# Kernel optimization log

Hardware: AMD Instinct MI355X
Metric: run time of the kernel (lower is better)

## Reference

```python
import jax, jax.numpy as jnp
import numpy as np

H = 32  # hidden size, fixed by the source module


def setup_inputs() -> dict:
    key = jax.random.key(0)
    ks = jax.random.split(key, 11)
    B, T = 1024, 999
    s = 0.1  # weight init scale
    return {
        "input": jax.random.normal(ks[0], (B, T), jnp.float32),
        "W_ih1": jax.random.normal(ks[1], (4 * H, 1), jnp.float32) * s,
        "W_hh1": jax.random.normal(ks[2], (4 * H, H), jnp.float32) * s,
        "b_ih1": jax.random.normal(ks[3], (4 * H,), jnp.float32) * s,
        "b_hh1": jax.random.normal(ks[4], (4 * H,), jnp.float32) * s,
        "W_ih2": jax.random.normal(ks[5], (4 * H, H), jnp.float32) * s,
        "W_hh2": jax.random.normal(ks[6], (4 * H, H), jnp.float32) * s,
        "b_ih2": jax.random.normal(ks[7], (4 * H,), jnp.float32) * s,
        "b_hh2": jax.random.normal(ks[8], (4 * H,), jnp.float32) * s,
        "W_lin": jax.random.normal(ks[9], (1, H), jnp.float32) * s,
        "b_lin": jax.random.normal(ks[10], (1,), jnp.float32) * s,
        "future": 1000,
    }


def _lstm_cell(x, h, c, W_ih, W_hh, b_ih, b_hh):
    # PyTorch LSTMCell: gates = x@W_ih^T + b_ih + h@W_hh^T + b_hh, order i,f,g,o
    z = x @ W_ih.T + h @ W_hh.T + (b_ih + b_hh)
    i, f, g, o = jnp.split(z, 4, axis=-1)
    c_new = jax.nn.sigmoid(f) * c + jax.nn.sigmoid(i) * jnp.tanh(g)
    h_new = jax.nn.sigmoid(o) * jnp.tanh(c_new)
    return h_new, c_new


def reference(input, W_ih1, W_hh1, b_ih1, b_hh1, W_ih2, W_hh2, b_ih2, b_hh2,
              W_lin, b_lin, future):
    B = input.shape[0]
    dt = input.dtype
    z = jnp.zeros((B, H), dt)

    def step_tf(carry, x_t):  # teacher-forced phase, x_t: [B]
        h1, c1, h2, c2 = carry
        h1, c1 = _lstm_cell(x_t[:, None], h1, c1, W_ih1, W_hh1, b_ih1, b_hh1)
        h2, c2 = _lstm_cell(h1, h2, c2, W_ih2, W_hh2, b_ih2, b_hh2)
        out = h2 @ W_lin.T + b_lin  # [B,1]
        return (h1, c1, h2, c2), out[:, 0]

    carry, outs1 = jax.lax.scan(step_tf, (z, z, z, z), input.T)  # outs1: [T,B]

    def step_gen(carry, _):
        h1, c1, h2, c2, out = carry
        h1, c1 = _lstm_cell(out, h1, c1, W_ih1, W_hh1, b_ih1, b_hh1)
        h2, c2 = _lstm_cell(h1, h2, c2, W_ih2, W_hh2, b_ih2, b_hh2)
        out = h2 @ W_lin.T + b_lin
        return (h1, c1, h2, c2, out), out[:, 0]

    last_out = outs1[-1][:, None]
    _, outs2 = jax.lax.scan(step_gen, (*carry, last_out), None, length=future)

    return jnp.concatenate([outs1, outs2], axis=0).T  # [B, T+future]
```

## Files before the change

kernel.cpp:

```cpp
#include <hip/hip_runtime.h>

#define HH 32
#define LOG2E 1.44269504088896340736f
#define KCH 16

typedef float v2f __attribute__((ext_vector_type(2)));

#define DPPF(v, ctrl) \
    __int_as_float(__builtin_amdgcn_update_dpp(0, __float_as_int(v), (ctrl), 0xF, 0xF, true))
#define QP_B0 0x00
#define QP_B1 0x55
#define QP_B2 0xAA
#define QP_B3 0xFF
#define DPP_ROR4  0x124
#define DPP_ROR8  0x128
#define SWZ(v, pat) __int_as_float(__builtin_amdgcn_ds_swizzle(__float_as_int(v), (pat)))

__device__ __forceinline__ float hw_exp2(float x) {
    float r; asm("v_exp_f32 %0, %1" : "=v"(r) : "v"(x)); return r;
}
__device__ __forceinline__ float sigm_e(float z, float e) {
    return __builtin_amdgcn_rcpf(1.0f + hw_exp2(z * e));
}
__device__ __forceinline__ v2f pk_fma(v2f a, v2f b, v2f c) {
    return __builtin_elementwise_fma(a, b, c);
}
__device__ __forceinline__ void load_bc(const float* p, v2f* d) {
#pragma unroll
    for (int r = 0; r < 8; ++r) {
        float4 v = ((const float4*)p)[r];
        d[2*r]   = (v2f){v.x, v.y};
        d[2*r+1] = (v2f){v.z, v.w};
    }
}
__device__ __forceinline__ float out_reduce(float p) {
    p += DPPF(p, DPP_ROR4);
    p += DPPF(p, DPP_ROR8);
    p += SWZ(p, 0x401F);
    p += __shfl_xor(p, 32, 64);
    return p;
}

__global__ __launch_bounds__(128, 2)
void lstm_seq_kernel(const float* __restrict__ input,
                     const float* __restrict__ W_ih1, const float* __restrict__ W_hh1,
                     const float* __restrict__ b_ih1, const float* __restrict__ b_hh1,
                     const float* __restrict__ W_ih2, const float* __restrict__ W_hh2,
                     const float* __restrict__ b_ih2, const float* __restrict__ b_hh2,
                     const float* __restrict__ W_lin, const float* __restrict__ b_lin,
                     float* __restrict__ out, int T, int total)
{
    const int b    = blockIdx.x;
    const int tid  = threadIdx.x;
    const int w    = tid >> 6;
    const int lane = tid & 63;
    const int q    = lane & 3;
    const int ch   = lane >> 2;
    const int rowA = (q << 5) | ch;
    const int rowB = (q << 5) | (ch + 16);

    __shared__ __align__(16) float ring[2 * KCH * HH];
    __shared__ __align__(16) float h1x[HH];
    __shared__ __align__(16) float h2s[HH];
    __shared__ float xbuf;

    const bool  isg = (q == 2);
    const float es  = isg ? (-2.0f * LOG2E) : (-LOG2E);
    const float mm  = isg ? 2.0f : 1.0f;
    const float cc  = isg ? -1.0f : 0.0f;

    v2f m1A[16], m1B[16], m2A[16], m2B[16];
    float wxA = 0.f, wxB = 0.f, bA, bB, wlA = 0.f, wlB = 0.f, blin = 0.f;
    if (w == 0) {
        const v2f* pA = (const v2f*)(W_hh1 + rowA * HH);
        const v2f* pB = (const v2f*)(W_hh1 + rowB * HH);
#pragma unroll
        for (int r = 0; r < 16; ++r) { m1A[r] = pA[r]; m1B[r] = pB[r]; }
        wxA = W_ih1[rowA]; wxB = W_ih1[rowB];
        bA  = b_ih1[rowA] + b_hh1[rowA];
        bB  = b_ih1[rowB] + b_hh1[rowB];
    } else {
        const v2f* pA = (const v2f*)(W_ih2 + rowA * HH);
        const v2f* pB = (const v2f*)(W_ih2 + rowB * HH);
        const v2f* qA = (const v2f*)(W_hh2 + rowA * HH);
        const v2f* qB = (const v2f*)(W_hh2 + rowB * HH);
#pragma unroll
        for (int r = 0; r < 16; ++r) { m1A[r] = pA[r]; m1B[r] = pB[r];
                                       m2A[r] = qA[r]; m2B[r] = qB[r]; }
        bA  = b_ih2[rowA] + b_hh2[rowA];
        bB  = b_ih2[rowB] + b_hh2[rowB];
        wlA = W_lin[ch]; wlB = W_lin[ch + 16]; blin = b_lin[0];
    }

    float cA = 0.f, cB = 0.f;
    v2f p0 = {0.f,0.f}, p1 = {0.f,0.f}, p2 = {0.f,0.f}, p3 = {0.f,0.f};

    const float* __restrict__ inp  = input + (size_t)b * T;
    float* __restrict__       outp = out   + (size_t)b * total;

    if (w == 0) {
        int t = 0;
        float xcur = inp[0];
        for (int cb = 0; t < T; ++cb) {
            float* buf = ring + (cb & 1) * (KCH * HH);
            int S = T - t; if (S > KCH) S = KCH;
            for (int s = 0; s < S; ++s, ++t) {
                float x = xcur;
                int tn = t + 1;
                xcur = inp[tn < T ? tn : 0];
                float z1A = fmaf(x, wxA, bA + (p0.x + p0.y) + (p1.x + p1.y));
                float z1B = fmaf(x, wxB, bB + (p2.x + p2.y) + (p3.x + p3.y));
                float acA = fmaf(mm, sigm_e(z1A, es), cc);
                float acB = fmaf(mm, sigm_e(z1B, es), cc);
                float iA = DPPF(acA, QP_B0), fA = DPPF(acA, QP_B1);
                float gA = DPPF(acA, QP_B2), oA = DPPF(acA, QP_B3);
                float iB = DPPF(acB, QP_B0), fB = DPPF(acB, QP_B1);
                float gB = DPPF(acB, QP_B2), oB = DPPF(acB, QP_B3);
                cA = fmaf(fA, cA, iA * gA);
                cB = fmaf(fB, cB, iB * gB);
                float hA = oA * fmaf(2.0f, sigm_e(cA, -2.0f * LOG2E), -1.0f);
                float hB = oB * fmaf(2.0f, sigm_e(cB, -2.0f * LOG2E), -1.0f);
                float* slot = buf + s * HH;
                if (q == 0) { slot[ch] = hA; slot[ch + 16] = hB; }
                v2f hv[16]; load_bc(slot, hv);
                p0 = (v2f){0.f,0.f}; p1 = (v2f){0.f,0.f};
                p2 = (v2f){0.f,0.f}; p3 = (v2f){0.f,0.f};
#pragma unroll
                for (int r = 0; r < 16; r += 2) {
                    p0 = pk_fma(hv[r],   m1A[r],   p0);
                    p1 = pk_fma(hv[r+1], m1A[r+1], p1);
                    p2 = pk_fma(hv[r],   m1B[r],   p2);
                    p3 = pk_fma(hv[r+1], m1B[r+1], p3);
                }
            }
            __syncthreads();
        }
        __syncthreads();
    } else {
        __syncthreads();
        int t = 0;
        for (int cb = 0; t < T; ++cb) {
            const float* buf = ring + (cb & 1) * (KCH * HH);
            int S = T - t; if (S > KCH) S = KCH;
            for (int s = 0; s < S; ++s, ++t) {
                v2f hv[16]; load_bc(buf + s * HH, hv);
                v2f s0 = p0, s1 = p1, s2 = p2, s3 = p3;
#pragma unroll
                for (int r = 0; r < 16; r += 2) {
                    s0 = pk_fma(hv[r],   m1A[r],   s0);
                    s1 = pk_fma(hv[r+1], m1A[r+1], s1);
                    s2 = pk_fma(hv[r],   m1B[r],   s2);
                    s3 = pk_fma(hv[r+1], m1B[r+1], s3);
                }
                float z2A = bA + (s0.x + s0.y) + (s1.x + s1.y);
                float z2B = bB + (s2.x + s2.y) + (s3.x + s3.y);
                float acA = fmaf(mm, sigm_e(z2A, es), cc);
                float acB = fmaf(mm, sigm_e(z2B, es), cc);
                float iA = DPPF(acA, QP_B0), fA = DPPF(acA, QP_B1);
                float gA = DPPF(acA, QP_B2), oA = DPPF(acA, QP_B3);
                float iB = DPPF(acB, QP_B0), fB = DPPF(acB, QP_B1);
                float gB = DPPF(acB, QP_B2), oB = DPPF(acB, QP_B3);
                cA = fmaf(fA, cA, iA * gA);
                cB = fmaf(fB, cB, iB * gB);
                float hA = oA * fmaf(2.0f, sigm_e(cA, -2.0f * LOG2E), -1.0f);
                float hB = oB * fmaf(2.0f, sigm_e(cB, -2.0f * LOG2E), -1.0f);
                if (q == 0) { h2s[ch] = hA; h2s[ch + 16] = hB; }
                v2f gv[16]; load_bc(h2s, gv);
                p0 = (v2f){0.f,0.f}; p1 = (v2f){0.f,0.f};
                p2 = (v2f){0.f,0.f}; p3 = (v2f){0.f,0.f};
#pragma unroll
                for (int r = 0; r < 16; r += 2) {
                    p0 = pk_fma(gv[r],   m2A[r],   p0);
                    p1 = pk_fma(gv[r+1], m2A[r+1], p1);
                    p2 = pk_fma(gv[r],   m2B[r],   p2);
                    p3 = pk_fma(gv[r+1], m2B[r+1], p3);
                }
                float pr = fmaf(hA, wlA, hB * wlB);
                float ov = out_reduce(pr) + blin;
                if (lane == 0) { outp[t] = ov; xbuf = ov; }
            }
            __syncthreads();
        }
    }

    for (int t = T; t < total; ++t) {
        __syncthreads();
        if (w == 0) {
            float x = xbuf;
            float z1A = fmaf(x, wxA, bA + (p0.x + p0.y) + (p1.x + p1.y));
            float z1B = fmaf(x, wxB, bB + (p2.x + p2.y) + (p3.x + p3.y));
            float acA = fmaf(mm, sigm_e(z1A, es), cc);
            float acB = fmaf(mm, sigm_e(z1B, es), cc);
            float iA = DPPF(acA, QP_B0), fA = DPPF(acA, QP_B1);
            float gA = DPPF(acA, QP_B2), oA = DPPF(acA, QP_B3);
            float iB = DPPF(acB, QP_B0), fB = DPPF(acB, QP_B1);
            float gB = DPPF(acB, QP_B2), oB = DPPF(acB, QP_B3);
            cA = fmaf(fA, cA, iA * gA);
            cB = fmaf(fB, cB, iB * gB);
            float hA = oA * fmaf(2.0f, sigm_e(cA, -2.0f * LOG2E), -1.0f);
            float hB = oB * fmaf(2.0f, sigm_e(cB, -2.0f * LOG2E), -1.0f);
            if (q == 0) { h1x[ch] = hA; h1x[ch + 16] = hB; }
        } else {
            v2f gv[16]; load_bc(h2s, gv);
            p0 = (v2f){0.f,0.f}; p1 = (v2f){0.f,0.f};
            p2 = (v2f){0.f,0.f}; p3 = (v2f){0.f,0.f};
#pragma unroll
            for (int r = 0; r < 16; r += 2) {
                p0 = pk_fma(gv[r],   m2A[r],   p0);
                p1 = pk_fma(gv[r+1], m2A[r+1], p1);
                p2 = pk_fma(gv[r],   m2B[r],   p2);
                p3 = pk_fma(gv[r+1], m2B[r+1], p3);
            }
        }
        __syncthreads();
        if (w == 0) {
            v2f hv[16]; load_bc(h1x, hv);
            p0 = (v2f){0.f,0.f}; p1 = (v2f){0.f,0.f};
            p2 = (v2f){0.f,0.f}; p3 = (v2f){0.f,0.f};
#pragma unroll
            for (int r = 0; r < 16; r += 2) {
                p0 = pk_fma(hv[r],   m1A[r],   p0);
                p1 = pk_fma(hv[r+1], m1A[r+1], p1);
                p2 = pk_fma(hv[r],   m1B[r],   p2);
                p3 = pk_fma(hv[r+1], m1B[r+1], p3);
            }
        } else {
            v2f hv[16]; load_bc(h1x, hv);
            v2f s0 = p0, s1 = p1, s2 = p2, s3 = p3;
#pragma unroll
            for (int r = 0; r < 16; r += 2) {
                s0 = pk_fma(hv[r],   m1A[r],   s0);
                s1 = pk_fma(hv[r+1], m1A[r+1], s1);
                s2 = pk_fma(hv[r],   m1B[r],   s2);
                s3 = pk_fma(hv[r+1], m1B[r+1], s3);
            }
            float z2A = bA + (s0.x + s0.y) + (s1.x + s1.y);
            float z2B = bB + (s2.x + s2.y) + (s3.x + s3.y);
            float acA = fmaf(mm, sigm_e(z2A, es), cc);
            float acB = fmaf(mm, sigm_e(z2B, es), cc);
            float iA = DPPF(acA, QP_B0), fA = DPPF(acA, QP_B1);
            float gA = DPPF(acA, QP_B2), oA = DPPF(acA, QP_B3);
            float iB = DPPF(acB, QP_B0), fB = DPPF(acB, QP_B1);
            float gB = DPPF(acB, QP_B2), oB = DPPF(acB, QP_B3);
            cA = fmaf(fA, cA, iA * gA);
            cB = fmaf(fB, cB, iB * gB);
            float hA = oA * fmaf(2.0f, sigm_e(cA, -2.0f * LOG2E), -1.0f);
            float hB = oB * fmaf(2.0f, sigm_e(cB, -2.0f * LOG2E), -1.0f);
            if (q == 0) { h2s[ch] = hA; h2s[ch + 16] = hB; }
            float pr = fmaf(hA, wlA, hB * wlB);
            float ov = out_reduce(pr) + blin;
            if (lane == 0) { outp[t] = ov; xbuf = ov; }
        }
    }
}

extern "C" void kernel_launch(void* const* d_in, const int* in_sizes, int n_in,
                              void* d_out, int out_size, void* d_ws, size_t ws_size,
                              hipStream_t stream) {
    const int B = 1024;
    const int T = in_sizes[0] / B;
    const int total = out_size / B;

    lstm_seq_kernel<<<dim3(B), dim3(128), 0, stream>>>(
        (const float*)d_in[0],
        (const float*)d_in[1], (const float*)d_in[2],
        (const float*)d_in[3], (const float*)d_in[4],
        (const float*)d_in[5], (const float*)d_in[6],
        (const float*)d_in[7], (const float*)d_in[8],
        (const float*)d_in[9], (const float*)d_in[10],
        (float*)d_out, T, total);
}
```

Before: 1.209 ms.

## Run generation phase in a single wave, removing per-step block barriers

Wave 0 now hands its final layer-1 pre-activations and cell state to wave 1 through shared memory and exits after the teacher-forced phase. Wave 1 then runs both LSTM layers of the autoregressive phase alone, so the two __syncthreads per future step are gone. The output reduction now uses DPP row broadcasts plus a readlane, so every lane gets the value without an LDS round trip. The teacher-forced consumer also prefetches the next ring slot during the current dot product. The cost is that wave 1 must hold four weight sets (m1, m2, m3) in registers, which raises register pressure and may spill, and the second half of the run has only one active wave per block.

```diff
diff --git a/kernel.cpp b/kernel.cpp
--- a/kernel.cpp
+++ b/kernel.cpp
@@ -12,9 +12,10 @@
 #define QP_B1 0x55
 #define QP_B2 0xAA
 #define QP_B3 0xFF
-#define DPP_ROR4  0x124
-#define DPP_ROR8  0x128
-#define SWZ(v, pat) __int_as_float(__builtin_amdgcn_ds_swizzle(__float_as_int(v), (pat)))
+#define ROR4  0x124
+#define ROR8  0x128
+#define BC15  0x142
+#define BC31  0x143
 
 __device__ __forceinline__ float hw_exp2(float x) {
     float r; asm("v_exp_f32 %0, %1" : "=v"(r) : "v"(x)); return r;
@@ -33,12 +34,35 @@
         d[2*r+1] = (v2f){v.z, v.w};
     }
 }
-__device__ __forceinline__ float out_reduce(float p) {
-    p += DPPF(p, DPP_ROR4);
-    p += DPPF(p, DPP_ROR8);
-    p += SWZ(p, 0x401F);
-    p += __shfl_xor(p, 32, 64);
-    return p;
+__device__ __forceinline__ float chan_reduce(float p) {
+    p += DPPF(p, ROR4);
+    p += DPPF(p, ROR8);
+    p += DPPF(p, BC15);
+    p += DPPF(p, BC31);
+    return __int_as_float(__builtin_amdgcn_readlane(__float_as_int(p), 63));
+}
+__device__ __forceinline__ void gates(float zA, float zB, float es, float mm, float cc,
+                                      float& cSA, float& cSB, float& hA, float& hB) {
+    float acA = fmaf(mm, sigm_e(zA, es), cc);
+    float acB = fmaf(mm, sigm_e(zB, es), cc);
+    float iA = DPPF(acA, QP_B0), fA = DPPF(acA, QP_B1);
+    float gA = DPPF(acA, QP_B2), oA = DPPF(acA, QP_B3);
+    float iB = DPPF(acB, QP_B0), fB = DPPF(acB, QP_B1);
+    float gB = DPPF(acB, QP_B2), oB = DPPF(acB, QP_B3);
+    cSA = fmaf(fA, cSA, iA * gA);
+    cSB = fmaf(fB, cSB, iB * gB);
+    hA = oA * fmaf(2.0f, sigm_e(cSA, -2.0f * LOG2E), -1.0f);
+    hB = oB * fmaf(2.0f, sigm_e(cSB, -2.0f * LOG2E), -1.0f);
+}
+__device__ __forceinline__ void dot16(const v2f* h, const v2f* mA, const v2f* mB,
+                                      v2f& r0, v2f& r1, v2f& r2, v2f& r3) {
+#pragma unroll
+    for (int r = 0; r < 16; r += 2) {
+        r0 = pk_fma(h[r],   mA[r],   r0);
+        r1 = pk_fma(h[r+1], mA[r+1], r1);
+        r2 = pk_fma(h[r],   mB[r],   r2);
+        r3 = pk_fma(h[r+1], mB[r+1], r3);
+    }
 }
 
 __global__ __launch_bounds__(128, 2)
@@ -60,47 +84,34 @@
     const int rowB = (q << 5) | (ch + 16);
 
     __shared__ __align__(16) float ring[2 * KCH * HH];
-    __shared__ __align__(16) float h1x[HH];
+    __shared__ __align__(16) float h1s[HH];
     __shared__ __align__(16) float h2s[HH];
-    __shared__ float xbuf;
+    __shared__ __align__(16) float zbuf[128];
+    __shared__ __align__(16) float cbuf[HH];
 
     const bool  isg = (q == 2);
     const float es  = isg ? (-2.0f * LOG2E) : (-LOG2E);
     const float mm  = isg ? 2.0f : 1.0f;
     const float cc  = isg ? -1.0f : 0.0f;
 
-    v2f m1A[16], m1B[16], m2A[16], m2B[16];
-    float wxA = 0.f, wxB = 0.f, bA, bB, wlA = 0.f, wlB = 0.f, blin = 0.f;
-    if (w == 0) {
-        const v2f* pA = (const v2f*)(W_hh1 + rowA * HH);
-        const v2f* pB = (const v2f*)(W_hh1 + rowB * HH);
-#pragma unroll
-        for (int r = 0; r < 16; ++r) { m1A[r] = pA[r]; m1B[r] = pB[r]; }
-        wxA = W_ih1[rowA]; wxB = W_ih1[rowB];
-        bA  = b_ih1[rowA] + b_hh1[rowA];
-        bB  = b_ih1[rowB] + b_hh1[rowB];
-    } else {
-        const v2f* pA = (const v2f*)(W_ih2 + rowA * HH);
-        const v2f* pB = (const v2f*)(W_ih2 + rowB * HH);
-        const v2f* qA = (const v2f*)(W_hh2 + rowA * HH);
-        const v2f* qB = (const v2f*)(W_hh2 + rowB * HH);
-#pragma unroll
-        for (int r = 0; r < 16; ++r) { m1A[r] = pA[r]; m1B[r] = pB[r];
-                                       m2A[r] = qA[r]; m2B[r] = qB[r]; }
-        bA  = b_ih2[rowA] + b_hh2[rowA];
-        bB  = b_ih2[rowB] + b_hh2[rowB];
-        wlA = W_lin[ch]; wlB = W_lin[ch + 16]; blin = b_lin[0];
-    }
-
-    float cA = 0.f, cB = 0.f;
-    v2f p0 = {0.f,0.f}, p1 = {0.f,0.f}, p2 = {0.f,0.f}, p3 = {0.f,0.f};
-
     const float* __restrict__ inp  = input + (size_t)b * T;
     float* __restrict__       outp = out   + (size_t)b * total;
 
     if (w == 0) {
+        v2f m1A[16], m1B[16];
+        {
+            const v2f* pA = (const v2f*)(W_hh1 + rowA * HH);
+            const v2f* pB = (const v2f*)(W_hh1 + rowB * HH);
+#pragma unroll
+            for (int r = 0; r < 16; ++r) { m1A[r] = pA[r]; m1B[r] = pB[r]; }
+        }
+        const float wxA = W_ih1[rowA], wxB = W_ih1[rowB];
+        const float bA  = b_ih1[rowA] + b_hh1[rowA];
+        const float bB  = b_ih1[rowB] + b_hh1[rowB];
+        float cA = 0.f, cB = 0.f;
+        v2f p0 = {0,0}, p1 = {0,0}, p2 = {0,0}, p3 = {0,0};
+        float xcur = inp[0];
         int t = 0;
-        float xcur = inp[0];
         for (int cb = 0; t < T; ++cb) {
             float* buf = ring + (cb & 1) * (KCH * HH);
             int S = T - t; if (S > KCH) S = KCH;
@@ -110,147 +121,104 @@
                 xcur = inp[tn < T ? tn : 0];
                 float z1A = fmaf(x, wxA, bA + (p0.x + p0.y) + (p1.x + p1.y));
                 float z1B = fmaf(x, wxB, bB + (p2.x + p2.y) + (p3.x + p3.y));
-                float acA = fmaf(mm, sigm_e(z1A, es), cc);
-                float acB = fmaf(mm, sigm_e(z1B, es), cc);
-                float iA = DPPF(acA, QP_B0), fA = DPPF(acA, QP_B1);
-                float gA = DPPF(acA, QP_B2), oA = DPPF(acA, QP_B3);
-                float iB = DPPF(acB, QP_B0), fB = DPPF(acB, QP_B1);
-                float gB = DPPF(acB, QP_B2), oB = DPPF(acB, QP_B3);
-                cA = fmaf(fA, cA, iA * gA);
-                cB = fmaf(fB, cB, iB * gB);
-                float hA = oA * fmaf(2.0f, sigm_e(cA, -2.0f * LOG2E), -1.0f);
-                float hB = oB * fmaf(2.0f, sigm_e(cB, -2.0f * LOG2E), -1.0f);
+                float hA, hB;
+                gates(z1A, z1B, es, mm, cc, cA, cB, hA, hB);
                 float* slot = buf + s * HH;
                 if (q == 0) { slot[ch] = hA; slot[ch + 16] = hB; }
                 v2f hv[16]; load_bc(slot, hv);
-                p0 = (v2f){0.f,0.f}; p1 = (v2f){0.f,0.f};
-                p2 = (v2f){0.f,0.f}; p3 = (v2f){0.f,0.f};
-#pragma unroll
-                for (int r = 0; r < 16; r += 2) {
-                    p0 = pk_fma(hv[r],   m1A[r],   p0);
-                    p1 = pk_fma(hv[r+1], m1A[r+1], p1);
-                    p2 = pk_fma(hv[r],   m1B[r],   p2);
-                    p3 = pk_fma(hv[r+1], m1B[r+1], p3);
-                }
+                p0 = (v2f){0,0}; p1 = (v2f){0,0}; p2 = (v2f){0,0}; p3 = (v2f){0,0};
+                dot16(hv, m1A, m1B, p0, p1, p2, p3);
             }
             __syncthreads();
         }
+        zbuf[lane]      = bA + (p0.x + p0.y) + (p1.x + p1.y);
+        zbuf[64 + lane] = bB + (p2.x + p2.y) + (p3.x + p3.y);
+        if (q == 0) { cbuf[ch] = cA; cbuf[16 + ch] = cB; }
         __syncthreads();
-    } else {
-        __syncthreads();
-        int t = 0;
-        for (int cb = 0; t < T; ++cb) {
-            const float* buf = ring + (cb & 1) * (KCH * HH);
-            int S = T - t; if (S > KCH) S = KCH;
-            for (int s = 0; s < S; ++s, ++t) {
-                v2f hv[16]; load_bc(buf + s * HH, hv);
-                v2f s0 = p0, s1 = p1, s2 = p2, s3 = p3;
-#pragma unroll
-                for (int r = 0; r < 16; r += 2) {
-                    s0 = pk_fma(hv[r],   m1A[r],   s0);
-                    s1 = pk_fma(hv[r+1], m1A[r+1], s1);
-                    s2 = pk_fma(hv[r],   m1B[r],   s2);
-                    s3 = pk_fma(hv[r+1], m1B[r+1], s3);
-                }
-                float z2A = bA + (s0.x + s0.y) + (s1.x + s1.y);
-                float z2B = bB + (s2.x + s2.y) + (s3.x + s3.y);
-                float acA = fmaf(mm, sigm_e(z2A, es), cc);
-                float acB = fmaf(mm, sigm_e(z2B, es), cc);
-                float iA = DPPF(acA, QP_B0), fA = DPPF(acA, QP_B1);
-                float gA = DPPF(acA, QP_B2), oA = DPPF(acA, QP_B3);
-                float iB = DPPF(acB, QP_B0), fB = DPPF(acB, QP_B1);
-                float gB = DPPF(acB, QP_B2), oB = DPPF(acB, QP_B3);
-                cA = fmaf(fA, cA, iA * gA);
-                cB = fmaf(fB, cB, iB * gB);
-                float hA = oA * fmaf(2.0f, sigm_e(cA, -2.0f * LOG2E), -1.0f);
-                float hB = oB * fmaf(2.0f, sigm_e(cB, -2.0f * LOG2E), -1.0f);
-                if (q == 0) { h2s[ch] = hA; h2s[ch + 16] = hB; }
-                v2f gv[16]; load_bc(h2s, gv);
-                p0 = (v2f){0.f,0.f}; p1 = (v2f){0.f,0.f};
-                p2 = (v2f){0.f,0.f}; p3 = (v2f){0.f,0.f};
-#pragma unroll
-                for (int r = 0; r < 16; r += 2) {
-                    p0 = pk_fma(gv[r],   m2A[r],   p0);
-                    p1 = pk_fma(gv[r+1], m2A[r+1], p1);
-                    p2 = pk_fma(gv[r],   m2B[r],   p2);
-                    p3 = pk_fma(gv[r+1], m2B[r+1], p3);
-                }
-                float pr = fmaf(hA, wlA, hB * wlB);
-                float ov = out_reduce(pr) + blin;
-                if (lane == 0) { outp[t] = ov; xbuf = ov; }
-            }
-            __syncthreads();
-        }
-    }
-
-    for (int t = T; t < total; ++t) {
-        __syncthreads();
-        if (w == 0) {
-            float x = xbuf;
-            float z1A = fmaf(x, wxA, bA + (p0.x + p0.y) + (p1.x + p1.y));
-            float z1B = fmaf(x, wxB, bB + (p2.x + p2.y) + (p3.x + p3.y));
-            float acA = fmaf(mm, sigm_e(z1A, es), cc);
-            float acB = fmaf(mm, sigm_e(z1B, es), cc);
-            float iA = DPPF(acA, QP_B0), fA = DPPF(acA, QP_B1);
-            float gA = DPPF(acA, QP_B2), oA = DPPF(acA, QP_B3);
-            float iB = DPPF(acB, QP_B0), fB = DPPF(acB, QP_B1);
-            float gB = DPPF(acB, QP_B2), oB = DPPF(acB, QP_B3);
-            cA = fmaf(fA, cA, iA * gA);
-            cB = fmaf(fB, cB, iB * gB);
-            float hA = oA * fmaf(2.0f, sigm_e(cA, -2.0f * LOG2E), -1.0f);
-            float hB = oB * fmaf(2.0f, sigm_e(cB, -2.0f * LOG2E), -1.0f);
-            if (q == 0) { h1x[ch] = hA; h1x[ch + 16] = hB; }
-        } else {
+        return;
+    }
+
+    v2f m1A[16], m1B[16], m2A[16], m2B[16];
+    {
+        const v2f* pA = (const v2f*)(W_ih2 + rowA * HH);
+        const v2f* pB = (const v2f*)(W_ih2 + rowB * HH);
+        const v2f* qA = (const v2f*)(W_hh2 + rowA * HH);
+        const v2f* qB = (const v2f*)(W_hh2 + rowB * HH);
+#pragma unroll
+        for (int r = 0; r < 16; ++r) { m1A[r] = pA[r]; m1B[r] = pB[r];
+                                       m2A[r] = qA[r]; m2B[r] = qB[r]; }
+    }
+    const float bA  = b_ih2[rowA] + b_hh2[rowA];
+    const float bB  = b_ih2[rowB] + b_hh2[rowB];
+    const float wlA = W_lin[ch], wlB = W_lin[ch + 16], blin = b_lin[0];
+
+    float cA = 0.f, cB = 0.f;
+    v2f p0 = {0,0}, p1 = {0,0}, p2 = {0,0}, p3 = {0,0};
+    float ov_s = 0.0f;
+
+    __syncthreads();
+    int t = 0;
+    for (int cb = 0; t < T; ++cb) {
+        const float* buf = ring + (cb & 1) * (KCH * HH);
+        int S = T - t; if (S > KCH) S = KCH;
+        v2f hv[16]; load_bc(buf, hv);
+        for (int s = 0; s < S; ++s, ++t) {
+            v2f s0 = p0, s1 = p1, s2 = p2, s3 = p3;
+            dot16(hv, m1A, m1B, s0, s1, s2, s3);
+            if (s + 1 < S) load_bc(buf + (s + 1) * HH, hv);
+            float z2A = bA + (s0.x + s0.y) + (s1.x + s1.y);
+            float z2B = bB + (s2.x + s2.y) + (s3.x + s3.y);
+            float hA, hB;
+            gates(z2A, z2B, es, mm, cc, cA, cB, hA, hB);
+            if (q == 0) { h2s[ch] = hA; h2s[ch + 16] = hB; }
             v2f gv[16]; load_bc(h2s, gv);
-            p0 = (v2f){0.f,0.f}; p1 = (v2f){0.f,0.f};
-            p2 = (v2f){0.f,0.f}; p3 = (v2f){0.f,0.f};
-#pragma unroll
-            for (int r = 0; r < 16; r += 2) {
-                p0 = pk_fma(gv[r],   m2A[r],   p0);
-                p1 = pk_fma(gv[r+1], m2A[r+1], p1);
-                p2 = pk_fma(gv[r],   m2B[r],   p2);
-                p3 = pk_fma(gv[r+1], m2B[r+1], p3);
-            }
+            float pr = fmaf(hA, wlA, hB * wlB);
+            ov_s = chan_reduce(pr) + blin;
+            if (lane == 0) outp[t] = ov_s;
+            p0 = (v2f){0,0}; p1 = (v2f){0,0}; p2 = (v2f){0,0}; p3 = (v2f){0,0};
+            dot16(gv, m2A, m2B, p0, p1, p2, p3);
         }
         __syncthreads();
-        if (w == 0) {
-            v2f hv[16]; load_bc(h1x, hv);
-            p0 = (v2f){0.f,0.f}; p1 = (v2f){0.f,0.f};
-            p2 = (v2f){0.f,0.f}; p3 = (v2f){0.f,0.f};
-#pragma unroll
-            for (int r = 0; r < 16; r += 2) {
-                p0 = pk_fma(hv[r],   m1A[r],   p0);
-                p1 = pk_fma(hv[r+1], m1A[r+1], p1);
-                p2 = pk_fma(hv[r],   m1B[r],   p2);
-                p3 = pk_fma(hv[r+1], m1B[r+1], p3);
-            }
-        } else {
-            v2f hv[16]; load_bc(h1x, hv);
-            v2f s0 = p0, s1 = p1, s2 = p2, s3 = p3;
-#pragma unroll
-            for (int r = 0; r < 16; r += 2) {
-                s0 = pk_fma(hv[r],   m1A[r],   s0);
-                s1 = pk_fma(hv[r+1], m1A[r+1], s1);
-                s2 = pk_fma(hv[r],   m1B[r],   s2);
-                s3 = pk_fma(hv[r+1], m1B[r+1], s3);
-            }
-            float z2A = bA + (s0.x + s0.y) + (s1.x + s1.y);
-            float z2B = bB + (s2.x + s2.y) + (s3.x + s3.y);
-            float acA = fmaf(mm, sigm_e(z2A, es), cc);
-            float acB = fmaf(mm, sigm_e(z2B, es), cc);
-            float iA = DPPF(acA, QP_B0), fA = DPPF(acA, QP_B1);
-            float gA = DPPF(acA, QP_B2), oA = DPPF(acA, QP_B3);
-            float iB = DPPF(acB, QP_B0), fB = DPPF(acB, QP_B1);
-            float gB = DPPF(acB, QP_B2), oB = DPPF(acB, QP_B3);
-            cA = fmaf(fA, cA, iA * gA);
-            cB = fmaf(fB, cB, iB * gB);
-            float hA = oA * fmaf(2.0f, sigm_e(cA, -2.0f * LOG2E), -1.0f);
-            float hB = oB * fmaf(2.0f, sigm_e(cB, -2.0f * LOG2E), -1.0f);
-            if (q == 0) { h2s[ch] = hA; h2s[ch + 16] = hB; }
-            float pr = fmaf(hA, wlA, hB * wlB);
-            float ov = out_reduce(pr) + blin;
-            if (lane == 0) { outp[t] = ov; xbuf = ov; }
-        }
+    }
+
+    v2f m3A[16], m3B[16];
+    {
+        const v2f* pA = (const v2f*)(W_hh1 + rowA * HH);
+        const v2f* pB = (const v2f*)(W_hh1 + rowB * HH);
+#pragma unroll
+        for (int r = 0; r < 16; ++r) { m3A[r] = pA[r]; m3B[r] = pB[r]; }
+    }
+    const float wxA = W_ih1[rowA], wxB = W_ih1[rowB];
+    const float b1A = b_ih1[rowA] + b_hh1[rowA];
+    const float b1B = b_ih1[rowB] + b_hh1[rowB];
+    float aA  = zbuf[lane], aB = zbuf[64 + lane];
+    float c1A = cbuf[ch],  c1B = cbuf[16 + ch];
+
+    for (int t2 = T; t2 < total; ++t2) {
+        float x = ov_s;
+        float z1A = fmaf(x, wxA, aA);
+        float z1B = fmaf(x, wxB, aB);
+        float h1A, h1B;
+        gates(z1A, z1B, es, mm, cc, c1A, c1B, h1A, h1B);
+        if (q == 0) { h1s[ch] = h1A; h1s[ch + 16] = h1B; }
+        v2f hv[16]; load_bc(h1s, hv);
+        v2f s0 = p0, s1 = p1, s2 = p2, s3 = p3;
+        dot16(hv, m1A, m1B, s0, s1, s2, s3);
+        v2f q0 = {0,0}, q1 = {0,0}, q2 = {0,0}, q3 = {0,0};
+        dot16(hv, m3A, m3B, q0, q1, q2, q3);
+        aA = b1A + (q0.x + q0.y) + (q1.x + q1.y);
+        aB = b1B + (q2.x + q2.y) + (q3.x + q3.y);
+        float z2A = bA + (s0.x + s0.y) + (s1.x + s1.y);
+        float z2B = bB + (s2.x + s2.y) + (s3.x + s3.y);
+        float h2A, h2B;
+        gates(z2A, z2B, es, mm, cc, cA, cB, h2A, h2B);
+        if (q == 0) { h2s[ch] = h2A; h2s[ch + 16] = h2B; }
+        v2f gv[16]; load_bc(h2s, gv);
+        float pr = fmaf(h2A, wlA, h2B * wlB);
+        ov_s = chan_reduce(pr) + blin;
+        if (lane == 0) outp[t2] = ov_s;
+        p0 = (v2f){0,0}; p1 = (v2f){0,0}; p2 = (v2f){0,0}; p3 = (v2f){0,0};
+        dot16(gv, m2A, m2B, p0, p1, p2, p3);
     }
 }
 
```

Result: slower. 2.382 ms (+97.0%).
